# Performance work log

Measured on AMD Instinct MI355X. Metric: run time of the kernel, lower is better.

The kernel has to match this reference:

```python
import jax, jax.numpy as jnp
import numpy as np

N = 50000
E = 800000
G_DIM = 512
H1 = 128
H2 = 128
R = 8  # 2 * n_speakers**2


def setup_inputs() -> dict:
    key = jax.random.key(0)
    ks = jax.random.split(key, 16)
    s = lambda d: 1.0 / np.sqrt(d)
    inp = {
        'node_features': jax.random.normal(ks[0], (N, G_DIM), jnp.float32),
        'edge_index': jax.random.randint(ks[1], (2, E), 0, N, jnp.int64),
        'edge_type': jax.random.randint(ks[2], (E,), 0, R, jnp.int64),
        # RGCNConv params
        'W_rel': jax.random.normal(ks[3], (R, G_DIM, H1), jnp.float32) * s(G_DIM),
        'W_root': jax.random.normal(ks[4], (G_DIM, H1), jnp.float32) * s(G_DIM),
        'b1': jnp.zeros((H1,), jnp.float32),
        # TransformerConv params (heads=1)
        'Wq': jax.random.normal(ks[5], (H1, H2), jnp.float32) * s(H1),
        'bq': jnp.zeros((H2,), jnp.float32),
        'Wk': jax.random.normal(ks[6], (H1, H2), jnp.float32) * s(H1),
        'bk': jnp.zeros((H2,), jnp.float32),
        'Wv': jax.random.normal(ks[7], (H1, H2), jnp.float32) * s(H1),
        'bv': jnp.zeros((H2,), jnp.float32),
        'Wskip': jax.random.normal(ks[8], (H1, H2), jnp.float32) * s(H1),
        'bskip': jnp.zeros((H2,), jnp.float32),
        # BatchNorm1d params
        'gamma': jnp.ones((H2,), jnp.float32),
        'beta': jnp.zeros((H2,), jnp.float32),
    }
    return inp


def reference(node_features, edge_index, edge_type, W_rel, W_root, b1,
              Wq, bq, Wk, bk, Wv, bv, Wskip, bskip, gamma, beta):
    n = node_features.shape[0]
    r = W_rel.shape[0]
    src, dst = edge_index[0], edge_index[1]

    # ---- RGCNConv: per-relation mean aggregation + root + bias ----
    # x @ W_r for all relations, then per-edge gather: [n,r,h1] -> [E,h1]
    xW = jnp.einsum('nf,rfh->nrh', node_features, W_rel)
    msg = xW[src, edge_type]                         # [E, H1]
    comp = dst * r + edge_type                       # composite (node, relation) key
    cnt = jax.ops.segment_sum(jnp.ones((msg.shape[0],), msg.dtype), comp,
                              num_segments=n * r)
    denom = jnp.maximum(cnt[comp], 1.0)[:, None]     # mean within each (node, rel)
    agg1 = jax.ops.segment_sum(msg / denom, dst, num_segments=n)
    h = agg1 + node_features @ W_root + b1           # [n, H1]

    # ---- TransformerConv (heads=1): segment-softmax attention ----
    q = h @ Wq + bq
    k = h @ Wk + bk
    v = h @ Wv + bv
    d = q.shape[-1]
    score = jnp.sum(q[dst] * k[src], axis=-1) / jnp.sqrt(jnp.float32(d))  # [E]
    smax = jax.ops.segment_max(score, dst, num_segments=n)
    smax = jnp.where(jnp.isfinite(smax), smax, 0.0)
    ex = jnp.exp(score - smax[dst])
    ssum = jax.ops.segment_sum(ex, dst, num_segments=n)
    alpha = ex / jnp.maximum(ssum[dst], 1e-16)       # [E]
    agg2 = jax.ops.segment_sum(alpha[:, None] * v[src], dst, num_segments=n)
    h2 = agg2 + h @ Wskip + bskip                    # root (lin_skip) path

    # ---- BatchNorm1d (training mode: batch stats) + LeakyReLU(0.01) ----
    mu = jnp.mean(h2, axis=0)
    var = jnp.mean((h2 - mu) ** 2, axis=0)
    xn = (h2 - mu) / jnp.sqrt(var + 1e-5)
    out = gamma * xn + beta
    return jnp.where(out >= 0, out, 0.01 * out)
```

## Files before the change

### kernel.cpp

```cpp
#include <hip/hip_runtime.h>

typedef float f32x4 __attribute__((ext_vector_type(4)));
typedef _Float16 f16x8 __attribute__((ext_vector_type(8)));
typedef _Float16 f16x2 __attribute__((ext_vector_type(2)));

#define NN 50000
#define EE 800000
#define GD 512
#define H1C 128
#define RR 8
#define NC1 1152
#define NC2 512
#define NCAST (NN * GD / 4)
#define PREPN (NCAST + NC1 * GD + NC2 * H1C)
#define MAXDEG 64

__device__ __forceinline__ unsigned short f2h(float f){
  _Float16 h = (_Float16)f;
  unsigned short u; __builtin_memcpy(&u, &h, 2); return u;
}
__device__ __forceinline__ float h2f(unsigned short u){
  _Float16 h; __builtin_memcpy(&h, &u, 2); return (float)h;
}
__device__ __forceinline__ void gload16(const void* g, void* l){
  __builtin_amdgcn_global_load_lds(
      (const __attribute__((address_space(1))) unsigned int*)g,
      (__attribute__((address_space(3))) unsigned int*)l, 16, 0, 0);
}
__device__ __forceinline__ float dot2(f16x2 a, f16x2 b, float c){
#if __has_builtin(__builtin_amdgcn_fdot2)
  return __builtin_amdgcn_fdot2(a, b, c, false);
#else
  return c + (float)a[0] * (float)b[0] + (float)a[1] * (float)b[1];
#endif
}

__global__ void k_zero(unsigned* __restrict__ zp, int n){
  int i = blockIdx.x * 256 + threadIdx.x;
  if (i < n) zp[i] = 0u;
}

__global__ void k_prep(const float* __restrict__ x, unsigned short* __restrict__ x16,
                       const float* __restrict__ W_rel, const float* __restrict__ W_root,
                       unsigned short* __restrict__ wcatT,
                       const float* __restrict__ Wq, const float* __restrict__ Wk,
                       const float* __restrict__ Wv, const float* __restrict__ Ws,
                       const float* __restrict__ bq, const float* __restrict__ bk,
                       const float* __restrict__ bv, const float* __restrict__ bs,
                       unsigned short* __restrict__ w2T, float* __restrict__ bias2,
                       const int* __restrict__ ei, const int* __restrict__ et,
                       int* __restrict__ deg, unsigned* __restrict__ srt){
  int i = blockIdx.x * 256 + threadIdx.x;
  if (i >= PREPN){
    int e = i - PREPN;
    if (e < EE){
      int dst = ei[EE + e];
      int pos = atomicAdd(&deg[dst], 1);
      if (pos < MAXDEG)
        srt[((size_t)dst << 6) + pos] = (unsigned)(ei[e] & 0xFFFF) | ((unsigned)et[e] << 16);
    }
    return;
  }
  if (i < NCAST){
    int b = i * 4;
    float4 v = *(const float4*)(x + b);
    ushort4 o;
    o.x = f2h(v.x); o.y = f2h(v.y); o.z = f2h(v.z); o.w = f2h(v.w);
    *(ushort4*)(x16 + b) = o;
    return;
  }
  i -= NCAST;
  if (i < NC1 * GD){
    int j = i >> 9;
    int f = i & 511;
    float v;
    if (j < 1024) v = W_rel[((size_t)(j >> 7) * GD + f) * H1C + (j & 127)];
    else          v = W_root[(size_t)f * H1C + (j - 1024)];
    wcatT[(size_t)j * GD + f] = f2h(v);
    return;
  }
  i -= NC1 * GD;
  if (i < NC2 * H1C){
    int j = i >> 7;
    int f = i & 127;
    int m = j >> 7;
    int hc = j & 127;
    const float* W = (m == 0) ? Wq : (m == 1) ? Wk : (m == 2) ? Wv : Ws;
    w2T[(size_t)j * H1C + f] = f2h(W[(size_t)f * H1C + hc]);
    if (f == 0){
      const float* B = (m == 0) ? bq : (m == 1) ? bk : (m == 2) ? bv : bs;
      bias2[j] = B[hc];
    }
  }
}

#define TILE 128
#define BK 64

__global__ __launch_bounds__(256) void k_gemm(
    const unsigned short* __restrict__ A,
    const unsigned short* __restrict__ Bt,
    unsigned short* __restrict__ C,
    const float* __restrict__ bias,
    int M, int Nout, int K, int rowsPerXcd, int colBlocks)
{
  int bid = blockIdx.x;
  int xcd = bid & 7;
  int lin = bid >> 3;
  int rowb = xcd * rowsPerXcd + lin / colBlocks;
  int colb = lin % colBlocks;
  int row0 = rowb * TILE;
  if (row0 >= M) return;
  int col0 = colb * TILE;

  __shared__ unsigned short As[TILE][BK];
  __shared__ unsigned short Bs[TILE][BK];
  int tid = threadIdx.x;
  int wave = tid >> 6, lane = tid & 63;
  int wm = (wave >> 1) * 64, wn = (wave & 1) * 64;
  int l16 = lane & 15, quad = lane >> 4;

  int srow = lane >> 3;
  int gcb  = ((lane & 7) ^ srow) * 8;
  int xorr = l16 & 7;

  f32x4 acc[4][4] = {};

  for (int k0 = 0; k0 < K; k0 += BK){
    __syncthreads();
    #pragma unroll
    for (int i = 0; i < 4; i++){
      int rbase = (wave * 4 + i) * 8;
      int gr = row0 + rbase + srow; if (gr >= M) gr = M - 1;
      gload16(A + (size_t)gr * K + k0 + gcb, &As[rbase][0]);
    }
    #pragma unroll
    for (int i = 0; i < 4; i++){
      int rbase = (wave * 4 + i) * 8;
      int gc = col0 + rbase + srow;
      gload16(Bt + (size_t)gc * K + k0 + gcb, &Bs[rbase][0]);
    }
    __syncthreads();
    #pragma unroll
    for (int ks = 0; ks < BK; ks += 32){
      int scol = ((quad + (ks >> 3)) ^ xorr) * 8;
      f16x8 af[4], bfr[4];
      #pragma unroll
      for (int i = 0; i < 4; i++) af[i] = *(const f16x8*)&As[wm + i*16 + l16][scol];
      #pragma unroll
      for (int j = 0; j < 4; j++) bfr[j] = *(const f16x8*)&Bs[wn + j*16 + l16][scol];
      #pragma unroll
      for (int i = 0; i < 4; i++)
        #pragma unroll
        for (int j = 0; j < 4; j++)
          acc[i][j] = __builtin_amdgcn_mfma_f32_16x16x32_f16(af[i], bfr[j], acc[i][j], 0, 0, 0);
    }
  }

  #pragma unroll
  for (int i = 0; i < 4; i++){
    int rbase = row0 + wm + i*16 + quad*4;
    #pragma unroll
    for (int j = 0; j < 4; j++){
      int col = col0 + wn + j*16 + l16;
      float b = bias ? bias[col] : 0.0f;
      #pragma unroll
      for (int rr = 0; rr < 4; rr++){
        int row = rbase + rr;
        if (row < M) C[(size_t)row * Nout + col] = f2h(acc[i][j][rr] + b);
      }
    }
  }
}

__global__ __launch_bounds__(256) void k_rgcn_seg(
    const int* __restrict__ deg, const unsigned* __restrict__ srt,
    const unsigned short* __restrict__ xW,
    const float* __restrict__ b1, unsigned short* __restrict__ h16)
{
  int v = blockIdx.x * 4 + (threadIdx.x >> 6);
  if (v >= NN) return;
  int lane = threadIdx.x & 63;
  int g = lane >> 4, l16 = lane & 15;
  int d = deg[v]; if (d > MAXDEG) d = MAXDEG;
  size_t start = (size_t)v << 6;

  unsigned long long c64 = 0;
  if (lane < d){
    unsigned sri = srt[start + lane];
    c64 = 1ull << ((sri >> 16) * 8);
  }
  #pragma unroll
  for (int off = 1; off < 64; off <<= 1) c64 += __shfl_xor(c64, off, 64);

  float o[8] = {};
  for (int cb = 0; cb < d; cb += 16){
    int srcs[4]; float invs[4];
    #pragma unroll
    for (int t = 0; t < 4; t++){
      int idx = cb + 4 * t + g;
      bool valid = idx < d;
      unsigned sri = valid ? srt[start + idx] : 0u;
      srcs[t] = (int)(sri & 0xFFFFu);
      int rel = (int)(sri >> 16);
      unsigned c = (unsigned)(c64 >> (rel * 8)) & 0xFFu;
      invs[t] = valid ? 1.0f / (float)c : 0.0f;
    }
    uint4 u[4];
    #pragma unroll
    for (int t = 0; t < 4; t++){
      int idx = cb + 4 * t + g;
      unsigned sri = (idx < d) ? srt[start + idx] : 0u;
      u[t] = *(const uint4*)(xW + (size_t)(sri & 0xFFFFu) * NC1 + (sri >> 16) * H1C + l16 * 8);
    }
    #pragma unroll
    for (int t = 0; t < 4; t++){
      const unsigned short* p = (const unsigned short*)&u[t];
      #pragma unroll
      for (int j = 0; j < 8; j++) o[j] += h2f(p[j]) * invs[t];
    }
  }
  #pragma unroll
  for (int j = 0; j < 8; j++){
    o[j] += __shfl_xor(o[j], 16, 64);
    o[j] += __shfl_xor(o[j], 32, 64);
  }
  if (g == 0){
    uint4 r = *(const uint4*)(xW + (size_t)v * NC1 + 1024 + l16 * 8);
    const unsigned short* p = (const unsigned short*)&r;
    unsigned short res[8];
    #pragma unroll
    for (int j = 0; j < 8; j++) res[j] = f2h(o[j] + h2f(p[j]) + b1[l16 * 8 + j]);
    *(uint4*)(h16 + (size_t)v * H1C + l16 * 8) = *(uint4*)res;
  }
}

__global__ __launch_bounds__(256) void k_attn3(
    const int* __restrict__ deg, const unsigned* __restrict__ srt,
    const unsigned short* __restrict__ qkvs, float* __restrict__ h2)
{
  int v = blockIdx.x * 4 + (threadIdx.x >> 6);
  if (v >= NN) return;
  int lane = threadIdx.x & 63;
  int g = lane >> 4, l16 = lane & 15;
  int d = deg[v]; if (d > MAXDEG) d = MAXDEG;
  size_t start = (size_t)v << 6;
  const float sc = 0.08838834764831845f;

  uint4 qa = *(const uint4*)(qkvs + (size_t)v * NC2 + l16 * 8);
  const f16x2* qh = (const f16x2*)&qa;

  float o[8] = {};
  float m = -INFINITY, l = 0.0f;

  for (int cb = 0; cb < d; cb += 16){
    int srcs[4]; bool val[4];
    #pragma unroll
    for (int t = 0; t < 4; t++){
      int idx = cb + 4 * t + g;
      val[t] = idx < d;
      srcs[t] = val[t] ? (int)(srt[start + idx] & 0xFFFFu) : 0;
    }
    uint4 ka[4], va[4];
    #pragma unroll
    for (int t = 0; t < 4; t++)
      ka[t] = *(const uint4*)(qkvs + (size_t)srcs[t] * NC2 + 128 + l16 * 8);
    #pragma unroll
    for (int t = 0; t < 4; t++)
      va[t] = *(const uint4*)(qkvs + (size_t)srcs[t] * NC2 + 256 + l16 * 8);

    float s[4];
    #pragma unroll
    for (int t = 0; t < 4; t++){
      const f16x2* kh = (const f16x2*)&ka[t];
      float ss = 0.0f;
      #pragma unroll
      for (int i = 0; i < 4; i++) ss = dot2(qh[i], kh[i], ss);
      #pragma unroll
      for (int off = 8; off >= 1; off >>= 1) ss += __shfl_xor(ss, off, 16);
      s[t] = val[t] ? ss * sc : -INFINITY;
    }

    float m4 = fmaxf(fmaxf(s[0], s[1]), fmaxf(s[2], s[3]));
    m4 = fmaxf(m4, __shfl_xor(m4, 16, 64));
    m4 = fmaxf(m4, __shfl_xor(m4, 32, 64));
    float newm = fmaxf(m, m4);
    float scale = __expf(m - newm);
    float e[4], esum = 0.0f;
    #pragma unroll
    for (int t = 0; t < 4; t++){
      e[t] = val[t] ? __expf(s[t] - newm) : 0.0f;
      esum += e[t];
    }
    esum += __shfl_xor(esum, 16, 64);
    esum += __shfl_xor(esum, 32, 64);
    l = l * scale + esum;

    #pragma unroll
    for (int j = 0; j < 8; j++) o[j] *= scale;
    #pragma unroll
    for (int t = 0; t < 4; t++){
      const unsigned short* p = (const unsigned short*)&va[t];
      #pragma unroll
      for (int j = 0; j < 8; j++) o[j] += e[t] * h2f(p[j]);
    }
    m = newm;
  }

  #pragma unroll
  for (int j = 0; j < 8; j++){
    o[j] += __shfl_xor(o[j], 16, 64);
    o[j] += __shfl_xor(o[j], 32, 64);
  }
  if (g == 0){
    float r = (d > 0) ? 1.0f / fmaxf(l, 1e-16f) : 0.0f;
    uint4 sk = *(const uint4*)(qkvs + (size_t)v * NC2 + 384 + l16 * 8);
    const unsigned short* p = (const unsigned short*)&sk;
    float* hd = h2 + (size_t)v * H1C + l16 * 8;
    float4 r0 = make_float4(h2f(p[0]) + o[0]*r, h2f(p[1]) + o[1]*r,
                            h2f(p[2]) + o[2]*r, h2f(p[3]) + o[3]*r);
    float4 r1 = make_float4(h2f(p[4]) + o[4]*r, h2f(p[5]) + o[5]*r,
                            h2f(p[6]) + o[6]*r, h2f(p[7]) + o[7]*r);
    *(float4*)hd = r0;
    *(float4*)(hd + 4) = r1;
  }
}

__global__ __launch_bounds__(256) void k_bn_reduce(const float* __restrict__ h2,
                                                   float* __restrict__ bn, int Nrows){
  __shared__ float ls[256], lq[256];
  int c = threadIdx.x & 127;
  int half = threadIdx.x >> 7;
  float s = 0.0f, q = 0.0f;
  for (int r = blockIdx.x * 2 + half; r < Nrows; r += gridDim.x * 2){
    float v = h2[(size_t)r * H1C + c];
    s += v; q += v * v;
  }
  ls[threadIdx.x] = s; lq[threadIdx.x] = q;
  __syncthreads();
  if (half == 0){
    atomicAdd(&bn[c],        ls[c] + ls[c + 128]);
    atomicAdd(&bn[128 + c],  lq[c] + lq[c + 128]);
  }
}

__global__ void k_out(const float* __restrict__ h2, const float* __restrict__ bn,
                      const float* __restrict__ gamma, const float* __restrict__ beta,
                      float* __restrict__ out, int n, float invN){
  int idx = blockIdx.x * blockDim.x + threadIdx.x;
  if (idx >= n) return;
  int c = idx & 127;
  float mu = bn[c] * invN;
  float var = bn[128 + c] * invN - mu * mu;
  float rs = rsqrtf(var + 1e-5f);
  float v = (h2[idx] - mu) * rs;
  float o = gamma[c] * v + beta[c];
  out[idx] = (o >= 0.0f) ? o : 0.01f * o;
}

extern "C" void kernel_launch(void* const* d_in, const int* in_sizes, int n_in,
                              void* d_out, int out_size, void* d_ws, size_t ws_size,
                              hipStream_t stream) {
  const float* x      = (const float*)d_in[0];
  const int*   ei     = (const int*)d_in[1];
  const int*   et     = (const int*)d_in[2];
  const float* W_rel  = (const float*)d_in[3];
  const float* W_root = (const float*)d_in[4];
  const float* b1     = (const float*)d_in[5];
  const float* Wq     = (const float*)d_in[6];
  const float* bq     = (const float*)d_in[7];
  const float* Wk     = (const float*)d_in[8];
  const float* bk     = (const float*)d_in[9];
  const float* Wv     = (const float*)d_in[10];
  const float* bv     = (const float*)d_in[11];
  const float* Wskip  = (const float*)d_in[12];
  const float* bskip  = (const float*)d_in[13];
  const float* gamma  = (const float*)d_in[14];
  const float* beta   = (const float*)d_in[15];
  float* out = (float*)d_out;

  const int N = NN, E = EE;
  char* ws = (char*)d_ws;
  size_t off = 0;
  auto alloc = [&](size_t bytes){ size_t r = off; off = (off + bytes + 255) & ~(size_t)255; return r; };

  size_t o_x16   = alloc((size_t)N * GD * 2);
  size_t o_w1    = alloc((size_t)NC1 * GD * 2);
  size_t o_xw    = alloc((size_t)N * NC1 * 2);
  size_t o_deg   = alloc((size_t)N * 4);
  size_t o_bn    = alloc((size_t)512 * 4);
  size_t o_zend  = off;
  size_t o_srt   = alloc((size_t)N * MAXDEG * 4);
  size_t o_h16   = alloc((size_t)N * H1C * 2);
  size_t o_w2    = alloc((size_t)NC2 * H1C * 2);
  size_t o_b2    = alloc((size_t)NC2 * 4);

  unsigned short* x16   = (unsigned short*)(ws + o_x16);
  unsigned short* qkvs  = (unsigned short*)(ws + o_x16);
  unsigned short* wcatT = (unsigned short*)(ws + o_w1);
  unsigned short* xW    = (unsigned short*)(ws + o_xw);
  float*          h2    = (float*)(ws + o_xw);
  int*            deg   = (int*)(ws + o_deg);
  float*          bn    = (float*)(ws + o_bn);
  unsigned*       srt   = (unsigned*)(ws + o_srt);
  unsigned short* h16   = (unsigned short*)(ws + o_h16);
  unsigned short* w2T   = (unsigned short*)(ws + o_w2);
  float*          bias2 = (float*)(ws + o_b2);

  const int TPB = 256;
  const int ROWB = (N + TILE - 1) / TILE;
  const int RPX  = (ROWB + 7) / 8;
  const int HISTB = (E + TPB - 1) / TPB;

  int nzero = (int)((o_zend - o_deg) / 4);
  k_zero<<<(nzero + TPB - 1) / TPB, TPB, 0, stream>>>((unsigned*)(ws + o_deg), nzero);

  k_prep<<<PREPN / TPB + HISTB, TPB, 0, stream>>>(
      x, x16, W_rel, W_root, wcatT,
      Wq, Wk, Wv, Wskip, bq, bk, bv, bskip, w2T, bias2,
      ei, et, deg, srt);

  k_gemm<<<8 * RPX * (NC1 / TILE), TPB, 0, stream>>>(x16, wcatT, xW, nullptr,
      N, NC1, GD, RPX, NC1 / TILE);

  k_rgcn_seg<<<(N + 3) / 4, TPB, 0, stream>>>(deg, srt, xW, b1, h16);

  k_gemm<<<8 * RPX * (NC2 / TILE), TPB, 0, stream>>>(h16, w2T, qkvs, bias2,
      N, NC2, H1C, RPX, NC2 / TILE);

  k_attn3<<<(N + 3) / 4, TPB, 0, stream>>>(deg, srt, qkvs, h2);

  k_bn_reduce<<<256, TPB, 0, stream>>>(h2, bn, N);
  k_out<<<((size_t)N * H1C + TPB - 1) / TPB, TPB, 0, stream>>>(h2, bn, gamma, beta, out, N * H1C, 1.0f / N);
}
```

Baseline: 524.0 us.

## Fuse fp32-to-fp16 input cast into first GEMM A-tile load

Removes the separate pass that converted node features to fp16 and instead has the first GEMM read fp32 rows, convert them in registers and write swizzled fp16 into LDS. This drops a write and reread of a 51 MB fp16 copy of the input. The trade is that this GEMM now reads 9 column tiles' worth of fp32 A (twice the bytes per tile) through plain loads plus conversion instead of async global-to-LDS loads. It also replaces the zeroing kernel with hipMemsetAsync and reuses the loaded edge entries in the RGCN aggregation instead of reloading them.

```diff
diff --git a/kernel.cpp b/kernel.cpp
--- a/kernel.cpp
+++ b/kernel.cpp
@@ -11,8 +11,7 @@
 #define RR 8
 #define NC1 1152
 #define NC2 512
-#define NCAST (NN * GD / 4)
-#define PREPN (NCAST + NC1 * GD + NC2 * H1C)
+#define PREPN2 (NC1 * GD + NC2 * H1C)
 #define MAXDEG 64
 
 __device__ __forceinline__ unsigned short f2h(float f){
@@ -35,13 +34,7 @@
 #endif
 }
 
-__global__ void k_zero(unsigned* __restrict__ zp, int n){
-  int i = blockIdx.x * 256 + threadIdx.x;
-  if (i < n) zp[i] = 0u;
-}
-
-__global__ void k_prep(const float* __restrict__ x, unsigned short* __restrict__ x16,
-                       const float* __restrict__ W_rel, const float* __restrict__ W_root,
+__global__ void k_prep(const float* __restrict__ W_rel, const float* __restrict__ W_root,
                        unsigned short* __restrict__ wcatT,
                        const float* __restrict__ Wq, const float* __restrict__ Wk,
                        const float* __restrict__ Wv, const float* __restrict__ Ws,
@@ -51,8 +44,8 @@
                        const int* __restrict__ ei, const int* __restrict__ et,
                        int* __restrict__ deg, unsigned* __restrict__ srt){
   int i = blockIdx.x * 256 + threadIdx.x;
-  if (i >= PREPN){
-    int e = i - PREPN;
+  if (i >= PREPN2){
+    int e = i - PREPN2;
     if (e < EE){
       int dst = ei[EE + e];
       int pos = atomicAdd(&deg[dst], 1);
@@ -61,15 +54,6 @@
     }
     return;
   }
-  if (i < NCAST){
-    int b = i * 4;
-    float4 v = *(const float4*)(x + b);
-    ushort4 o;
-    o.x = f2h(v.x); o.y = f2h(v.y); o.z = f2h(v.z); o.w = f2h(v.w);
-    *(ushort4*)(x16 + b) = o;
-    return;
-  }
-  i -= NCAST;
   if (i < NC1 * GD){
     int j = i >> 9;
     int f = i & 511;
@@ -97,8 +81,9 @@
 #define TILE 128
 #define BK 64
 
+template<int AF32>
 __global__ __launch_bounds__(256) void k_gemm(
-    const unsigned short* __restrict__ A,
+    const void* __restrict__ Ap,
     const unsigned short* __restrict__ Bt,
     unsigned short* __restrict__ C,
     const float* __restrict__ bias,
@@ -131,14 +116,38 @@
     #pragma unroll
     for (int i = 0; i < 4; i++){
       int rbase = (wave * 4 + i) * 8;
-      int gr = row0 + rbase + srow; if (gr >= M) gr = M - 1;
-      gload16(A + (size_t)gr * K + k0 + gcb, &As[rbase][0]);
-    }
-    #pragma unroll
-    for (int i = 0; i < 4; i++){
-      int rbase = (wave * 4 + i) * 8;
       int gc = col0 + rbase + srow;
       gload16(Bt + (size_t)gc * K + k0 + gcb, &Bs[rbase][0]);
+    }
+    if constexpr (AF32){
+      const float* A32 = (const float*)Ap;
+      int rowi = tid >> 4;
+      int c16  = tid & 15;
+      float4 va[8];
+      #pragma unroll
+      for (int p = 0; p < 8; p++){
+        int gr = row0 + p * 16 + rowi; if (gr >= M) gr = M - 1;
+        va[p] = *(const float4*)(A32 + (size_t)gr * K + k0 + c16 * 4);
+      }
+      #pragma unroll
+      for (int p = 0; p < 8; p++){
+        int lr = p * 16 + rowi;
+        unsigned long long pk =
+              (unsigned long long)f2h(va[p].x)
+            | ((unsigned long long)f2h(va[p].y) << 16)
+            | ((unsigned long long)f2h(va[p].z) << 32)
+            | ((unsigned long long)f2h(va[p].w) << 48);
+        int col = (((c16 >> 1) ^ (lr & 7)) << 3) + (c16 & 1) * 4;
+        *(unsigned long long*)&As[lr][col] = pk;
+      }
+    } else {
+      const unsigned short* A16 = (const unsigned short*)Ap;
+      #pragma unroll
+      for (int i = 0; i < 4; i++){
+        int rbase = (wave * 4 + i) * 8;
+        int gr = row0 + rbase + srow; if (gr >= M) gr = M - 1;
+        gload16(A16 + (size_t)gr * K + k0 + gcb, &As[rbase][0]);
+      }
     }
     __syncthreads();
     #pragma unroll
@@ -195,24 +204,19 @@
 
   float o[8] = {};
   for (int cb = 0; cb < d; cb += 16){
-    int srcs[4]; float invs[4];
+    unsigned sris[4]; float invs[4];
     #pragma unroll
     for (int t = 0; t < 4; t++){
       int idx = cb + 4 * t + g;
       bool valid = idx < d;
-      unsigned sri = valid ? srt[start + idx] : 0u;
-      srcs[t] = (int)(sri & 0xFFFFu);
-      int rel = (int)(sri >> 16);
-      unsigned c = (unsigned)(c64 >> (rel * 8)) & 0xFFu;
+      sris[t] = valid ? srt[start + idx] : 0u;
+      unsigned c = (unsigned)(c64 >> ((sris[t] >> 16) * 8)) & 0xFFu;
       invs[t] = valid ? 1.0f / (float)c : 0.0f;
     }
     uint4 u[4];
     #pragma unroll
-    for (int t = 0; t < 4; t++){
-      int idx = cb + 4 * t + g;
-      unsigned sri = (idx < d) ? srt[start + idx] : 0u;
-      u[t] = *(const uint4*)(xW + (size_t)(sri & 0xFFFFu) * NC1 + (sri >> 16) * H1C + l16 * 8);
-    }
+    for (int t = 0; t < 4; t++)
+      u[t] = *(const uint4*)(xW + (size_t)(sris[t] & 0xFFFFu) * NC1 + (sris[t] >> 16) * H1C + l16 * 8);
     #pragma unroll
     for (int t = 0; t < 4; t++){
       const unsigned short* p = (const unsigned short*)&u[t];
@@ -384,7 +388,7 @@
   size_t off = 0;
   auto alloc = [&](size_t bytes){ size_t r = off; off = (off + bytes + 255) & ~(size_t)255; return r; };
 
-  size_t o_x16   = alloc((size_t)N * GD * 2);
+  size_t o_qkv   = alloc((size_t)N * NC2 * 2);
   size_t o_w1    = alloc((size_t)NC1 * GD * 2);
   size_t o_xw    = alloc((size_t)N * NC1 * 2);
   size_t o_deg   = alloc((size_t)N * 4);
@@ -395,8 +399,7 @@
   size_t o_w2    = alloc((size_t)NC2 * H1C * 2);
   size_t o_b2    = alloc((size_t)NC2 * 4);
 
-  unsigned short* x16   = (unsigned short*)(ws + o_x16);
-  unsigned short* qkvs  = (unsigned short*)(ws + o_x16);
+  unsigned short* qkvs  = (unsigned short*)(ws + o_qkv);
   unsigned short* wcatT = (unsigned short*)(ws + o_w1);
   unsigned short* xW    = (unsigned short*)(ws + o_xw);
   float*          h2    = (float*)(ws + o_xw);
@@ -412,20 +415,19 @@
   const int RPX  = (ROWB + 7) / 8;
   const int HISTB = (E + TPB - 1) / TPB;
 
-  int nzero = (int)((o_zend - o_deg) / 4);
-  k_zero<<<(nzero + TPB - 1) / TPB, TPB, 0, stream>>>((unsigned*)(ws + o_deg), nzero);
-
-  k_prep<<<PREPN / TPB + HISTB, TPB, 0, stream>>>(
-      x, x16, W_rel, W_root, wcatT,
+  hipMemsetAsync(ws + o_deg, 0, o_zend - o_deg, stream);
+
+  k_prep<<<PREPN2 / TPB + HISTB, TPB, 0, stream>>>(
+      W_rel, W_root, wcatT,
       Wq, Wk, Wv, Wskip, bq, bk, bv, bskip, w2T, bias2,
       ei, et, deg, srt);
 
-  k_gemm<<<8 * RPX * (NC1 / TILE), TPB, 0, stream>>>(x16, wcatT, xW, nullptr,
+  k_gemm<1><<<8 * RPX * (NC1 / TILE), TPB, 0, stream>>>(x, wcatT, xW, nullptr,
       N, NC1, GD, RPX, NC1 / TILE);
 
   k_rgcn_seg<<<(N + 3) / 4, TPB, 0, stream>>>(deg, srt, xW, b1, h16);
 
-  k_gemm<<<8 * RPX * (NC2 / TILE), TPB, 0, stream>>>(h16, w2T, qkvs, bias2,
+  k_gemm<0><<<8 * RPX * (NC2 / TILE), TPB, 0, stream>>>(h16, w2T, qkvs, bias2,
       N, NC2, H1C, RPX, NC2 / TILE);
 
   k_attn3<<<(N + 3) / 4, TPB, 0, stream>>>(deg, srt, qkvs, h2);
```

Measured after the change: 583.6 us. +11.4%, slower.
